# Performance work log

Hardware: AMD Instinct MI355X
Metric: run time of the kernel (lower is better)

Reference implementation:

```python
import jax, jax.numpy as jnp
import numpy as np

B = 8192          # batch of scenes
H = 20            # human_num
O = 10            # other_robot_num
IN = 13           # input_dim
SELF = 6          # self_state_dim
AG = IN - SELF    # agent_state_dim = 7
E1, E2 = 256, 128 # wr_dims / wh_dims
HID = 32          # hardcoded hidden_channels in Graphgnn
FIN = 128         # final_state_dim
P1, P2, P3 = 256, 128, 1  # planning_dims
NE = 8            # number of hetero edge types
# edge-type index convention:
# 0 robot->human, 1 human->robot, 2 other->robot, 3 robot->other,
# 4 other->human, 5 human->other, 6 human->human, 7 other->other


def setup_inputs() -> dict:
    key = jax.random.key(0)
    ks = iter(jax.random.split(key, 40))
    def nrm(shape, scale=0.05):
        return jax.random.normal(next(ks), shape, jnp.float32) * scale
    inp = {}
    inp["state"] = jax.random.normal(next(ks), (B, H + O, IN), jnp.float32)
    inp["dropout"] = 0  # unused by forward (kept for signature fidelity)
    # w_r: SELF -> E1 -> E2 (last_relu=True)
    inp["wr_W0"] = nrm((SELF, E1)); inp["wr_b0"] = nrm((E1,))
    inp["wr_W1"] = nrm((E1, E2));   inp["wr_b1"] = nrm((E2,))
    # w_h: AG -> E1 -> E2
    inp["wh_W0"] = nrm((AG, E1));   inp["wh_b0"] = nrm((E1,))
    inp["wh_W1"] = nrm((E1, E2));   inp["wh_b1"] = nrm((E2,))
    # w_o: AG -> E1 -> E2
    inp["wo_W0"] = nrm((AG, E1));   inp["wo_b0"] = nrm((E1,))
    inp["wo_W1"] = nrm((E1, E2));   inp["wo_b1"] = nrm((E2,))
    # per-edge-type GraphConv params (PyG GraphConv: lin_rel has bias, lin_root has none)
    inp["c1_relW"]  = nrm((NE, E2, HID)); inp["c1_relb"]  = nrm((NE, HID))
    inp["c1_rootW"] = nrm((NE, E2, HID))
    inp["c2_relW"]  = nrm((NE, HID, FIN)); inp["c2_relb"]  = nrm((NE, FIN))
    inp["c2_rootW"] = nrm((NE, HID, FIN))
    # value_net: FIN -> P1 -> P2 -> P3 (no final relu)
    inp["v_W0"] = nrm((FIN, P1)); inp["v_b0"] = nrm((P1,))
    inp["v_W1"] = nrm((P1, P2));  inp["v_b1"] = nrm((P2,))
    inp["v_W2"] = nrm((P2, P3));  inp["v_b2"] = nrm((P3,))
    return inp


def _mlp2(x, W0, b0, W1, b1, last_relu):
    h = jax.nn.relu(x @ W0 + b0)
    h = h @ W1 + b1
    return jax.nn.relu(h) if last_relu else h


def _hetero_conv(xr, xh, xo, relW, relb, rootW):
    # xr: [B,1,D], xh: [B,H,D], xo: [B,O,D]
    # GraphConv per edge type: out_dst = lin_root(x_dst) + lin_rel(sum of src messages)
    # graph is complete bipartite (sence) / complete-minus-self (affect),
    # so aggregations are closed-form sums.
    lin  = lambda x, i: jnp.einsum('bnd,do->bno', x, relW[i]) + relb[i]
    root = lambda x, i: jnp.einsum('bnd,do->bno', x, rootW[i])
    sh = xh.sum(axis=1, keepdims=True)  # [B,1,D] sum over humans
    so = xo.sum(axis=1, keepdims=True)  # [B,1,D] sum over other robots
    # robot receives: human->robot (1), other->robot (2)
    out_r = lin(sh, 1) + root(xr, 1) + lin(so, 2) + root(xr, 2)
    # human receives: robot->human (0), other->human (4), human->human (6)
    out_h = (lin(xr, 0) + root(xh, 0)
             + lin(so, 4) + root(xh, 4)
             + lin(sh - xh, 6) + root(xh, 6))
    # other receives: robot->other (3), human->other (5), other->other (7)
    out_o = (lin(xr, 3) + root(xo, 3)
             + lin(sh, 5) + root(xo, 5)
             + lin(so - xo, 7) + root(xo, 7))
    return out_r, out_h, out_o


def reference(state, dropout,
              wr_W0, wr_b0, wr_W1, wr_b1,
              wh_W0, wh_b0, wh_W1, wh_b1,
              wo_W0, wo_b0, wo_W1, wo_b1,
              c1_relW, c1_relb, c1_rootW,
              c2_relW, c2_relb, c2_rootW,
              v_W0, v_b0, v_W1, v_b1, v_W2, v_b2):
    self_state = state[:, 0, :SELF]          # [B, SELF]
    human_states = state[:, :H, SELF:]       # [B, H, AG]
    other_states = state[:, H:, SELF:]       # [B, O, AG]
    er = _mlp2(self_state, wr_W0, wr_b0, wr_W1, wr_b1, True)[:, None, :]  # [B,1,E2]
    eh = _mlp2(human_states, wh_W0, wh_b0, wh_W1, wh_b1, True)            # [B,H,E2]
    eo = _mlp2(other_states, wo_W0, wo_b0, wo_W1, wo_b1, True)            # [B,O,E2]
    r, h, o = _hetero_conv(er, eh, eo, c1_relW, c1_relb, c1_rootW)
    r, h, o = jax.nn.relu(r), jax.nn.relu(h), jax.nn.relu(o)
    r, h, o = _hetero_conv(r, h, o, c2_relW, c2_relb, c2_rootW)
    r = jax.nn.relu(r)
    hr = r[:, 0, :]                           # robot node per scene, [B, FIN]
    v = jax.nn.relu(hr @ v_W0 + v_b0)
    v = jax.nn.relu(v @ v_W1 + v_b1)
    v = v @ v_W2 + v_b2                       # [B, 1]
    return v
```

## Files before the change

kernel.cpp:

```cpp
#include <hip/hip_runtime.h>
#include <hip/hip_bf16.h>
#include <stdint.h>

#define BATCH 8192
#define NSTATE 30
#define DIN 13
#define E1 256
#define E2 128

typedef short bf16x8 __attribute__((ext_vector_type(8)));
typedef float f32x4 __attribute__((ext_vector_type(4)));
typedef __bf16 bf16x2_t __attribute__((ext_vector_type(2)));

__device__ __forceinline__ unsigned short f2b(float f) {
    return __builtin_bit_cast(unsigned short, (__bf16)f);
}
__device__ __forceinline__ float b2f(unsigned short b) {
    return __uint_as_float((unsigned)b << 16);
}
__device__ __forceinline__ unsigned pack2(float a, float b) {
    bf16x2_t v = {(__bf16)fmaxf(a, 0.f), (__bf16)fmaxf(b, 0.f)};
    return __builtin_bit_cast(unsigned, v);
}
__device__ __forceinline__ unsigned pack2n(float a, float b) {
    bf16x2_t v = {(__bf16)a, (__bf16)b};
    return __builtin_bit_cast(unsigned, v);
}

__device__ __forceinline__ bf16x8 pin_frag(bf16x8 v) {
    uint4 u = __builtin_bit_cast(uint4, v);
    asm volatile("" : "+v"(u.x), "+v"(u.y), "+v"(u.z), "+v"(u.w));
    return __builtin_bit_cast(bf16x8, u);
}
__device__ __forceinline__ f32x4 pin_f4(f32x4 v) {
    uint4 u = __builtin_bit_cast(uint4, v);
    asm volatile("" : "+v"(u.x), "+v"(u.y), "+v"(u.z), "+v"(u.w));
    return __builtin_bit_cast(f32x4, u);
}

__device__ __forceinline__ float wcat_val(int k, int m, const float* relW, const float* rootW) {
    int part = k >> 7, c = k & 127, grp = m >> 5, mm = m & 31;
    int off = c * 32 + mm;
    if (part == 0) return (grp == 0) ? rootW[4096 + off] + rootW[8192 + off]
                        : (grp == 1) ? relW[off] : relW[3*4096 + off];
    if (part == 1) return (grp == 0) ? relW[1*4096 + off]
                        : (grp == 1) ? relW[6*4096 + off] : relW[5*4096 + off];
    return (grp == 0) ? relW[2*4096 + off]
         : (grp == 1) ? relW[4*4096 + off] : relW[7*4096 + off];
}
__device__ __forceinline__ float wc2_val(int k, int n, const float* relW, const float* rootW) {
    int grp = k >> 5, kk = k & 31;
    int off = kk * 128 + n;
    if (grp == 0) return rootW[4096 + off] + rootW[8192 + off];
    if (grp == 1) return relW[4096 + off];
    return relW[8192 + off];
}

__global__ void k_prep(const float* __restrict__ c1_relW, const float* __restrict__ c1_relb,
                       const float* __restrict__ c1_rootW,
                       const float* __restrict__ c2_relW, const float* __restrict__ c2_relb,
                       const float* __restrict__ c2_rootW,
                       const float* __restrict__ wh_W0, const float* __restrict__ wh_W1,
                       const float* __restrict__ wo_W0, const float* __restrict__ wo_W1,
                       const float* __restrict__ wr_W0, const float* __restrict__ wr_W1,
                       const float* __restrict__ v_W0, const float* __restrict__ v_W1,
                       const float* __restrict__ b0h, const float* __restrict__ b0o,
                       const float* __restrict__ b0r,
                       float* __restrict__ bcat, float* __restrict__ bc2,
                       unsigned short* __restrict__ W0b_h, unsigned short* __restrict__ W0b_o,
                       unsigned short* __restrict__ W0b_r,
                       unsigned short* __restrict__ W1f_h, unsigned short* __restrict__ W1f_o,
                       unsigned short* __restrict__ W1f_r,
                       unsigned short* __restrict__ Mf_h, unsigned short* __restrict__ Mf_o,
                       unsigned short* __restrict__ Wcatf, unsigned short* __restrict__ Wc2f,
                       unsigned short* __restrict__ vW0f, unsigned short* __restrict__ vW1f)
{
    int gid = blockIdx.x * blockDim.x + threadIdx.x;
    int gsz = gridDim.x * blockDim.x;

    for (int i = gid; i < 96; i += gsz) {
        int grp = i >> 5, mm = i & 31;
        float v;
        if (grp == 0)      v = c1_relb[32 + mm] + c1_relb[64 + mm];
        else if (grp == 1) v = c1_relb[mm] + c1_relb[128 + mm] + c1_relb[192 + mm];
        else               v = c1_relb[96 + mm] + c1_relb[160 + mm] + c1_relb[224 + mm];
        bcat[i] = v;
    }
    for (int i = gid; i < 128; i += gsz) bc2[i] = c2_relb[128 + i] + c2_relb[256 + i];

    for (int i = gid; i < 2048; i += gsz) {
        int n = i >> 3, j = i & 7;
        W0b_h[i] = (j < 7) ? f2b(wh_W0[j * 256 + n]) : f2b(b0h[n]);
        W0b_o[i] = (j < 7) ? f2b(wo_W0[j * 256 + n]) : f2b(b0o[n]);
        W0b_r[i] = (j < 6) ? f2b(wr_W0[j * 256 + n])
                 : (j == 6) ? f2b(b0r[n]) : (unsigned short)0;
    }
    for (int i = gid; i < 32768; i += gsz) {
        int j = i & 7, l = (i >> 3) & 63, nt = (i >> 9) & 7, ks = i >> 12;
        int k = ks * 32 + (l >> 4) * 8 + j;
        int n = nt * 16 + (l & 15);
        W1f_h[i] = f2b(wh_W1[k * 128 + n]);
        W1f_o[i] = f2b(wo_W1[k * 128 + n]);
        W1f_r[i] = f2b(wr_W1[k * 128 + n]);
    }
    for (int i = gid; i < 4096; i += gsz) {
        int j = i & 7, l = (i >> 3) & 63, nt = (i >> 9) & 1, ks = i >> 10;
        int k = ks * 32 + (l >> 4) * 8 + j;
        int n = nt * 16 + (l & 15);
        int i0 = k * 32 + n;
        Mf_h[i] = f2b(c1_rootW[i0] + c1_rootW[4*4096 + i0] + c1_rootW[6*4096 + i0] - c1_relW[6*4096 + i0]);
        Mf_o[i] = f2b(c1_rootW[3*4096 + i0] + c1_rootW[5*4096 + i0] + c1_rootW[7*4096 + i0] - c1_relW[7*4096 + i0]);
    }
    for (int i = gid; i < 36864; i += gsz) {
        int j = i & 7, l = (i >> 3) & 63, rem = i >> 9;
        int nt = rem % 6, ks = rem / 6;
        int k = ks * 32 + (l >> 4) * 8 + j;
        int n = nt * 16 + (l & 15);
        Wcatf[i] = f2b(wcat_val(k, n, c1_relW, c1_rootW));
    }
    for (int i = gid; i < 12288; i += gsz) {
        int j = i & 7, l = (i >> 3) & 63, rem = i >> 9;
        int nt = rem & 7, ks = rem >> 3;
        int k = ks * 32 + (l >> 4) * 8 + j;
        int n = nt * 16 + (l & 15);
        Wc2f[i] = f2b(wc2_val(k, n, c2_relW, c2_rootW));
    }
    for (int i = gid; i < 32768; i += gsz) {
        int j = i & 7, l = (i >> 3) & 63, rem = i >> 9;
        int nt = rem & 15, ks = rem >> 4;
        int k = ks * 32 + (l >> 4) * 8 + j;
        int n = nt * 16 + (l & 15);
        vW0f[i] = f2b(v_W0[k * 256 + n]);
    }
    for (int i = gid; i < 32768; i += gsz) {
        int j = i & 7, l = (i >> 3) & 63, rem = i >> 9;
        int nt = rem & 7, ks = rem >> 3;
        int k = ks * 32 + (l >> 4) * 8 + j;
        int n = nt * 16 + (l & 15);
        vW1f[i] = f2b(v_W1[k * 128 + n]);
    }
}

#define SM_W0   0
#define SM_MF   4096
#define SM_W1   12288
#define SM_B1   78848
#define SM_HS   79360
#define SM_SZ   (79360 + 8 * 16 * 264 * 2)

template<int NPB, int NODE0, int INOFF, int INDIM, bool TAIL>
__device__ __forceinline__ void mlp_blockE(
    int blkrow0, const float* __restrict__ state,
    const unsigned short* __restrict__ W0b_g,
    const unsigned short* __restrict__ W1f_g, const float* __restrict__ b1,
    const unsigned short* __restrict__ Mf_g,
    unsigned short* __restrict__ tR, float* __restrict__ sumB,
    unsigned short* __restrict__ eR, char* smem)
{
    unsigned short* W0s = (unsigned short*)(smem + SM_W0);
    unsigned short* Mfs = (unsigned short*)(smem + SM_MF);
    unsigned short* W1s = (unsigned short*)(smem + SM_W1);
    float* b1s          = (float*)(smem + SM_B1);

    const int t = threadIdx.x;
    const int lane = t & 63;
    const int w = t >> 6;
    const int l15 = lane & 15;
    const int quad = lane >> 4;
    const int R0 = blkrow0 + w * 128;
    unsigned short* hw = (unsigned short*)(smem + SM_HS) + w * (16 * 264);
    unsigned short* ew = hw;

    if (t < 256) ((uint4*)W0s)[t] = ((const uint4*)W0b_g)[t];
    if (t >= 256 && t < 384) b1s[t - 256] = b1[t - 256];
    #pragma unroll
    for (int i = 0; i < 8; ++i)
        ((uint4*)W1s)[t + 512 * i] = ((const uint4*)W1f_g)[t + 512 * i];
    if constexpr (TAIL)
        ((uint4*)Mfs)[t] = ((const uint4*)Mf_g)[t];
    __syncthreads();

    bf16x8 wreg[32];
    #pragma unroll
    for (int ks = 0; ks < 8; ++ks)
        #pragma unroll
        for (int nt = 0; nt < 4; ++nt)
            wreg[ks * 4 + nt] =
                pin_frag(*(const bf16x8*)(W1s + ((ks * 8 + nt) * 64 + lane) * 8));

    f32x4 bias1[8];
    #pragma unroll
    for (int nt = 0; nt < 8; ++nt) {
        float4 bb = *(const float4*)(b1s + nt * 16 + quad * 4);
        bias1[nt] = pin_f4((f32x4){bb.x, bb.y, bb.z, bb.w});
    }

    float s0 = 0.f, s1 = 0.f;
    int bcur = R0 / NPB;

    float xf[INDIM];
    #pragma unroll 1
    for (int dummy = 0; dummy < 1; ++dummy) {
        if (quad == 0) {
            int grow = R0 + l15;
            int b = grow / NPB;
            int n = grow - b * NPB + NODE0;
            const float* xp = state + ((size_t)b * NSTATE + n) * DIN + INOFF;
            #pragma unroll
            for (int j = 0; j < INDIM; ++j) xf[j] = xp[j];
        }
    }

    for (int sub = 0; sub < 8; ++sub) {
        const int wrow0 = R0 + sub * 16;

        bf16x8 bx = {};
        if (quad == 0) {
            #pragma unroll
            for (int j = 0; j < INDIM; ++j)
                bx[j] = (short)f2b(xf[j]);
            bx[INDIM] = (short)0x3F80;
        }
        if (sub < 7 && quad == 0) {
            int grow = wrow0 + 16 + l15;
            int b = grow / NPB;
            int n = grow - b * NPB + NODE0;
            const float* xp = state + ((size_t)b * NSTATE + n) * DIN + INOFF;
            #pragma unroll
            for (int j = 0; j < INDIM; ++j) xf[j] = xp[j];
        }

        #pragma unroll
        for (int nt = 0; nt < 16; ++nt) {
            bf16x8 aw = {};
            if (quad == 0)
                aw = *(const bf16x8*)(W0s + (nt * 16 + l15) * 8);
            f32x4 c = {0.f, 0.f, 0.f, 0.f};
            c = __builtin_amdgcn_mfma_f32_16x16x32_bf16(aw, bx, c, 0, 0, 0);
            uint2 pv = {pack2(c[0], c[1]), pack2(c[2], c[3])};
            *(uint2*)(hw + l15 * 264 + nt * 16 + quad * 4) = pv;
        }

        f32x4 acc[8];
        #pragma unroll
        for (int nt = 0; nt < 8; ++nt) acc[nt] = bias1[nt];
        #pragma unroll
        for (int ks = 0; ks < 8; ++ks) {
            bf16x8 bh = *(const bf16x8*)(hw + l15 * 264 + ks * 32 + quad * 8);
            #pragma unroll
            for (int nt = 0; nt < 8; ++nt) {
                bf16x8 aw = (nt < 4)
                    ? wreg[ks * 4 + nt]
                    : *(const bf16x8*)(W1s + ((ks * 8 + nt) * 64 + lane) * 8);
                acc[nt] = __builtin_amdgcn_mfma_f32_16x16x32_bf16(aw, bh, acc[nt], 0, 0, 0);
            }
        }

        if constexpr (TAIL) {
            __asm__ __volatile__("s_waitcnt lgkmcnt(0)" ::: "memory");
            #pragma unroll
            for (int nt = 0; nt < 8; ++nt) {
                uint2 pv = {pack2(acc[nt][0], acc[nt][1]), pack2(acc[nt][2], acc[nt][3])};
                *(uint2*)(ew + l15 * 136 + nt * 16 + quad * 4) = pv;
            }

            f32x4 tacc[2] = {{0.f,0.f,0.f,0.f},{0.f,0.f,0.f,0.f}};
            #pragma unroll
            for (int ks = 0; ks < 4; ++ks) {
                bf16x8 ae = *(const bf16x8*)(ew + l15 * 136 + ks * 32 + quad * 8);
                #pragma unroll
                for (int nt = 0; nt < 2; ++nt) {
                    bf16x8 bm = *(const bf16x8*)(Mfs + ((ks * 2 + nt) * 64 + lane) * 8);
                    tacc[nt] = __builtin_amdgcn_mfma_f32_16x16x32_bf16(bm, ae, tacc[nt], 0, 0, 0);
                }
            }
            #pragma unroll
            for (int nt = 0; nt < 2; ++nt) {
                uint2 pv = {pack2n(tacc[nt][0], tacc[nt][1]), pack2n(tacc[nt][2], tacc[nt][3])};
                *(uint2*)(tR + (size_t)(wrow0 + l15) * 32 + nt * 16 + quad * 4) = pv;
            }

            #pragma unroll
            for (int r = 0; r < 16; ++r) {
                int b = (wrow0 + r) / NPB;
                if (b != bcur) {
                    bool interior = (bcur * NPB >= R0) && ((bcur + 1) * NPB <= R0 + 128);
                    float* dst = sumB + (size_t)bcur * 128 + 2 * lane;
                    if (interior) { dst[0] = s0; dst[1] = s1; }
                    else { atomicAdd(dst, s0); atomicAdd(dst + 1, s1); }
                    s0 = 0.f; s1 = 0.f; bcur = b;
                }
                unsigned v = *(const unsigned*)(ew + r * 136 + lane * 2);
                s0 += b2f((unsigned short)v);
                s1 += b2f((unsigned short)(v >> 16));
            }
            if (sub == 7) {
                bool interior = (bcur * NPB >= R0) && ((bcur + 1) * NPB <= R0 + 128);
                float* dst = sumB + (size_t)bcur * 128 + 2 * lane;
                if (interior) { dst[0] = s0; dst[1] = s1; }
                else { atomicAdd(dst, s0); atomicAdd(dst + 1, s1); }
            }
        } else {
            #pragma unroll
            for (int nt = 0; nt < 8; ++nt) {
                uint2 pv = {pack2(acc[nt][0], acc[nt][1]), pack2(acc[nt][2], acc[nt][3])};
                *(uint2*)(eR + (size_t)(wrow0 + l15) * 128 + nt * 16 + quad * 4) = pv;
            }
        }
        __asm__ __volatile__("" ::: "memory");
    }
}

__global__ __launch_bounds__(512, 2) void k_mlpE(
    const float* __restrict__ state,
    const unsigned short* __restrict__ W0b_h,
    const unsigned short* __restrict__ W1f_h, const float* __restrict__ b1_h,
    const unsigned short* __restrict__ Mf_h, unsigned short* __restrict__ tR_h,
    float* __restrict__ shB,
    const unsigned short* __restrict__ W0b_o,
    const unsigned short* __restrict__ W1f_o, const float* __restrict__ b1_o,
    const unsigned short* __restrict__ Mf_o, unsigned short* __restrict__ tR_o,
    float* __restrict__ soB,
    const unsigned short* __restrict__ W0b_r,
    const unsigned short* __restrict__ W1f_r, const float* __restrict__ b1_r,
    unsigned short* __restrict__ eR)
{
    __shared__ __align__(16) char smem[SM_SZ];
    int bid = blockIdx.x;
    if (bid < 160)
        mlp_blockE<20, 0, 6, 7, true>(bid * 1024, state, W0b_h, W1f_h, b1_h,
                                      Mf_h, tR_h, shB, nullptr, smem);
    else if (bid < 240)
        mlp_blockE<10, 20, 6, 7, true>((bid - 160) * 1024, state, W0b_o, W1f_o, b1_o,
                                       Mf_o, tR_o, soB, nullptr, smem);
    else
        mlp_blockE<1, 0, 0, 6, false>((bid - 240) * 1024, state, W0b_r, W1f_r, b1_r,
                                      nullptr, nullptr, nullptr, eR, smem);
}

__global__ __launch_bounds__(256, 2) void k_tail(
    const unsigned short* __restrict__ eR,
    const float* __restrict__ shB, const float* __restrict__ soB,
    const unsigned short* __restrict__ tR_h, const unsigned short* __restrict__ tR_o,
    const unsigned short* __restrict__ Wcatf, const float* __restrict__ bcat,
    const unsigned short* __restrict__ Wc2f, const float* __restrict__ bc2,
    const unsigned short* __restrict__ vW0f, const float* __restrict__ vb0,
    const unsigned short* __restrict__ vW1f, const float* __restrict__ vb1,
    const float* __restrict__ vW2, const float* __restrict__ vb2,
    float* __restrict__ out)
{
    __shared__ __align__(16) char sm[33024];
    unsigned short* Ub  = (unsigned short*)(sm);
    unsigned short* V1b = (unsigned short*)(sm);
    unsigned short* Vb  = (unsigned short*)(sm + 12800);
    float* chL          = (float*)(sm + 16128);
    float* coL          = (float*)(sm + 18176);
    unsigned short* Hb  = (unsigned short*)(sm + 20224);
    float* V2b          = (float*)(sm + 24576);

    const int t = threadIdx.x, lane = t & 63, w = t >> 6;
    const int l15 = lane & 15, quad = lane >> 4;
    const int b0 = blockIdx.x * 16;
    const int rowb = quad * 4;

    {
        int b = t >> 4, q = t & 15;
        ((uint4*)(Ub + b * 400))[q] = ((const uint4*)(eR + (size_t)(b0 + b) * 128))[q];
    }
    for (int idx = t; idx < 4096; idx += 256) {
        int b = idx >> 8, kk = idx & 255;
        float v = (kk < 128) ? shB[(size_t)(b0 + b) * 128 + kk]
                             : soB[(size_t)(b0 + b) * 128 + kk - 128];
        Ub[b * 400 + 128 + kk] = f2b(v);
    }
    __syncthreads();

    for (int nt = w; nt < 6; nt += 4) {
        float bias = bcat[nt * 16 + l15];
        f32x4 acc = {bias, bias, bias, bias};
        #pragma unroll
        for (int ks = 0; ks < 12; ++ks) {
            bf16x8 a = *(const bf16x8*)(Ub + l15 * 400 + ks * 32 + quad * 8);
            bf16x8 bw = *(const bf16x8*)(Wcatf + ((ks * 6 + nt) * 64 + lane) * 8);
            acc = __builtin_amdgcn_mfma_f32_16x16x32_bf16(a, bw, acc, 0, 0, 0);
        }
        int n = nt * 16 + l15;
        #pragma unroll
        for (int reg = 0; reg < 4; ++reg) {
            float v = acc[reg];
            int b = rowb + reg;
            if (n < 32)      Vb[b * 104 + n] = f2b(fmaxf(v, 0.f));
            else if (n < 64) chL[b * 32 + (n - 32)] = v;
            else             coL[b * 32 + (n - 64)] = v;
        }
    }
    __syncthreads();

    for (int idx = t; idx < 512; idx += 256) {
        int b = idx >> 5, m = idx & 31;
        float ch = chL[b * 32 + m];
        const unsigned short* p = tR_h + (size_t)(b0 + b) * 20 * 32 + m;
        float s = 0.f;
        #pragma unroll
        for (int n = 0; n < 20; ++n) s += fmaxf(ch + b2f(p[n * 32]), 0.f);
        Vb[b * 104 + 32 + m] = f2b(s);
        float co = coL[b * 32 + m];
        const unsigned short* p2 = tR_o + (size_t)(b0 + b) * 10 * 32 + m;
        float s2 = 0.f;
        #pragma unroll
        for (int n = 0; n < 10; ++n) s2 += fmaxf(co + b2f(p2[n * 32]), 0.f);
        Vb[b * 104 + 64 + m] = f2b(s2);
    }
    __syncthreads();

    {
        f32x4 acc[2];
        #pragma unroll
        for (int q = 0; q < 2; ++q) {
            int nt = w + q * 4;
            float bias = bc2[nt * 16 + l15];
            acc[q] = (f32x4){bias, bias, bias, bias};
        }
        #pragma unroll
        for (int ks = 0; ks < 3; ++ks) {
            bf16x8 a = *(const bf16x8*)(Vb + l15 * 104 + ks * 32 + quad * 8);
            #pragma unroll
            for (int q = 0; q < 2; ++q) {
                int nt = w + q * 4;
                bf16x8 bw = *(const bf16x8*)(Wc2f + ((ks * 8 + nt) * 64 + lane) * 8);
                acc[q] = __builtin_amdgcn_mfma_f32_16x16x32_bf16(a, bw, acc[q], 0, 0, 0);
            }
        }
        #pragma unroll
        for (int q = 0; q < 2; ++q) {
            int nt = w + q * 4;
            #pragma unroll
            for (int reg = 0; reg < 4; ++reg)
                Hb[(rowb + reg) * 136 + nt * 16 + l15] = f2b(fmaxf(acc[q][reg], 0.f));
        }
    }
    __syncthreads();

    {
        f32x4 acc[4];
        #pragma unroll
        for (int q = 0; q < 4; ++q) {
            int nt = w + q * 4;
            float bias = vb0[nt * 16 + l15];
            acc[q] = (f32x4){bias, bias, bias, bias};
        }
        #pragma unroll
        for (int ks = 0; ks < 4; ++ks) {
            bf16x8 a = *(const bf16x8*)(Hb + l15 * 136 + ks * 32 + quad * 8);
            #pragma unroll
            for (int q = 0; q < 4; ++q) {
                int nt = w + q * 4;
                bf16x8 bw = *(const bf16x8*)(vW0f + ((ks * 16 + nt) * 64 + lane) * 8);
                acc[q] = __builtin_amdgcn_mfma_f32_16x16x32_bf16(a, bw, acc[q], 0, 0, 0);
            }
        }
        __syncthreads();
        #pragma unroll
        for (int q = 0; q < 4; ++q) {
            int nt = w + q * 4;
            #pragma unroll
            for (int reg = 0; reg < 4; ++reg)
                V1b[(rowb + reg) * 264 + nt * 16 + l15] = f2b(fmaxf(acc[q][reg], 0.f));
        }
    }
    __syncthreads();

    {
        f32x4 acc[2];
        #pragma unroll
        for (int q = 0; q < 2; ++q) {
            int nt = w + q * 4;
            float bias = vb1[nt * 16 + l15];
            acc[q] = (f32x4){bias, bias, bias, bias};
        }
        #pragma unroll
        for (int ks = 0; ks < 8; ++ks) {
            bf16x8 a = *(const bf16x8*)(V1b + l15 * 264 + ks * 32 + quad * 8);
            #pragma unroll
            for (int q = 0; q < 2; ++q) {
                int nt = w + q * 4;
                bf16x8 bw = *(const bf16x8*)(vW1f + ((ks * 8 + nt) * 64 + lane) * 8);
                acc[q] = __builtin_amdgcn_mfma_f32_16x16x32_bf16(a, bw, acc[q], 0, 0, 0);
            }
        }
        #pragma unroll
        for (int q = 0; q < 2; ++q) {
            int nt = w + q * 4;
            #pragma unroll
            for (int reg = 0; reg < 4; ++reg)
                V2b[(rowb + reg) * 132 + nt * 16 + l15] = fmaxf(acc[q][reg], 0.f);
        }
    }
    __syncthreads();

    if (t < 128) {
        int b = t >> 3, j = t & 7;
        float v = 0.f;
        #pragma unroll
        for (int k = 0; k < 16; ++k)
            v = fmaf(V2b[b * 132 + j * 16 + k], vW2[j * 16 + k], v);
        v += __shfl_down(v, 4, 8);
        v += __shfl_down(v, 2, 8);
        v += __shfl_down(v, 1, 8);
        if (j == 0) out[b0 + b] = v + vb2[0];
    }
}

extern "C" void kernel_launch(void* const* d_in, const int* in_sizes, int n_in,
                              void* d_out, int out_size, void* d_ws, size_t ws_size,
                              hipStream_t stream)
{
    const float* state   = (const float*)d_in[0];
    const float* wr_W0   = (const float*)d_in[2];
    const float* wr_b0   = (const float*)d_in[3];
    const float* wr_W1   = (const float*)d_in[4];
    const float* wr_b1   = (const float*)d_in[5];
    const float* wh_W0   = (const float*)d_in[6];
    const float* wh_b0   = (const float*)d_in[7];
    const float* wh_W1   = (const float*)d_in[8];
    const float* wh_b1   = (const float*)d_in[9];
    const float* wo_W0   = (const float*)d_in[10];
    const float* wo_b0   = (const float*)d_in[11];
    const float* wo_W1   = (const float*)d_in[12];
    const float* wo_b1   = (const float*)d_in[13];
    const float* c1_relW = (const float*)d_in[14];
    const float* c1_relb = (const float*)d_in[15];
    const float* c1_rootW= (const float*)d_in[16];
    const float* c2_relW = (const float*)d_in[17];
    const float* c2_relb = (const float*)d_in[18];
    const float* c2_rootW= (const float*)d_in[19];
    const float* v_W0    = (const float*)d_in[20];
    const float* v_b0    = (const float*)d_in[21];
    const float* v_W1    = (const float*)d_in[22];
    const float* v_b1    = (const float*)d_in[23];
    const float* v_W2    = (const float*)d_in[24];
    const float* v_b2    = (const float*)d_in[25];

    char* ws = (char*)d_ws;
    size_t off = 0;
    auto alloc = [&](size_t bytes) -> char* {
        char* p = ws + off;
        off = (off + bytes + 255) & ~(size_t)255;
        return p;
    };
    float* shB  = (float*)alloc((size_t)BATCH * 128 * 4);
    float* soB  = (float*)alloc((size_t)BATCH * 128 * 4);
    unsigned short* tR_h = (unsigned short*)alloc((size_t)163840 * 32 * 2);
    unsigned short* tR_o = (unsigned short*)alloc((size_t)81920 * 32 * 2);
    unsigned short* eR   = (unsigned short*)alloc((size_t)BATCH * 128 * 2);
    float* bcat = (float*)alloc(96 * 4);
    float* bc2  = (float*)alloc(128 * 4);
    unsigned short* W0b_h = (unsigned short*)alloc(2048 * 2);
    unsigned short* W0b_o = (unsigned short*)alloc(2048 * 2);
    unsigned short* W0b_r = (unsigned short*)alloc(2048 * 2);
    unsigned short* W1f_h = (unsigned short*)alloc(32768 * 2);
    unsigned short* W1f_o = (unsigned short*)alloc(32768 * 2);
    unsigned short* W1f_r = (unsigned short*)alloc(32768 * 2);
    unsigned short* Mf_h  = (unsigned short*)alloc(4096 * 2);
    unsigned short* Mf_o  = (unsigned short*)alloc(4096 * 2);
    unsigned short* Wcatf = (unsigned short*)alloc(36864 * 2);
    unsigned short* Wc2f  = (unsigned short*)alloc(12288 * 2);
    unsigned short* vW0f  = (unsigned short*)alloc(32768 * 2);
    unsigned short* vW1f  = (unsigned short*)alloc(32768 * 2);
    (void)ws_size; (void)in_sizes; (void)n_in; (void)out_size;

    hipMemsetAsync(shB, 0, (size_t)2 * BATCH * 128 * 4, stream);

    k_prep<<<256, 256, 0, stream>>>(c1_relW, c1_relb, c1_rootW, c2_relW, c2_relb, c2_rootW,
                                    wh_W0, wh_W1, wo_W0, wo_W1, wr_W0, wr_W1, v_W0, v_W1,
                                    wh_b0, wo_b0, wr_b0,
                                    bcat, bc2, W0b_h, W0b_o, W0b_r, W1f_h, W1f_o, W1f_r,
                                    Mf_h, Mf_o, Wcatf, Wc2f, vW0f, vW1f);

    k_mlpE<<<248, 512, 0, stream>>>(state,
                                    W0b_h, W1f_h, wh_b1, Mf_h, tR_h, shB,
                                    W0b_o, W1f_o, wo_b1, Mf_o, tR_o, soB,
                                    W0b_r, W1f_r, wr_b1, eR);

    k_tail<<<512, 256, 0, stream>>>(eR, shB, soB, tR_h, tR_o,
                                    Wcatf, bcat, Wc2f, bc2, vW0f, v_b0, vW1f, v_b1,
                                    v_W2, v_b2, (float*)d_out);
}
```

Baseline: 169.7 us.

## Chain MFMA outputs through registers by permuting weight K-ordering

```diff
diff --git a/kernel.cpp b/kernel.cpp
--- a/kernel.cpp
+++ b/kernel.cpp
@@ -27,11 +27,6 @@
     return __builtin_bit_cast(unsigned, v);
 }
 
-__device__ __forceinline__ bf16x8 pin_frag(bf16x8 v) {
-    uint4 u = __builtin_bit_cast(uint4, v);
-    asm volatile("" : "+v"(u.x), "+v"(u.y), "+v"(u.z), "+v"(u.w));
-    return __builtin_bit_cast(bf16x8, u);
-}
 __device__ __forceinline__ f32x4 pin_f4(f32x4 v) {
     uint4 u = __builtin_bit_cast(uint4, v);
     asm volatile("" : "+v"(u.x), "+v"(u.y), "+v"(u.z), "+v"(u.w));
@@ -97,17 +92,17 @@
     }
     for (int i = gid; i < 32768; i += gsz) {
         int j = i & 7, l = (i >> 3) & 63, nt = (i >> 9) & 7, ks = i >> 12;
-        int k = ks * 32 + (l >> 4) * 8 + j;
+        int kk = ((j >> 2) * 8 + ks) * 16 + (l >> 4) * 4 + (j & 3);
         int n = nt * 16 + (l & 15);
-        W1f_h[i] = f2b(wh_W1[k * 128 + n]);
-        W1f_o[i] = f2b(wo_W1[k * 128 + n]);
-        W1f_r[i] = f2b(wr_W1[k * 128 + n]);
+        W1f_h[i] = f2b(wh_W1[kk * 128 + n]);
+        W1f_o[i] = f2b(wo_W1[kk * 128 + n]);
+        W1f_r[i] = f2b(wr_W1[kk * 128 + n]);
     }
     for (int i = gid; i < 4096; i += gsz) {
         int j = i & 7, l = (i >> 3) & 63, nt = (i >> 9) & 1, ks = i >> 10;
-        int k = ks * 32 + (l >> 4) * 8 + j;
+        int kk = ((j >> 2) * 4 + ks) * 16 + (l >> 4) * 4 + (j & 3);
         int n = nt * 16 + (l & 15);
-        int i0 = k * 32 + n;
+        int i0 = kk * 32 + n;
         Mf_h[i] = f2b(c1_rootW[i0] + c1_rootW[4*4096 + i0] + c1_rootW[6*4096 + i0] - c1_relW[6*4096 + i0]);
         Mf_o[i] = f2b(c1_rootW[3*4096 + i0] + c1_rootW[5*4096 + i0] + c1_rootW[7*4096 + i0] - c1_relW[7*4096 + i0]);
     }
@@ -144,9 +139,9 @@
 #define SM_W0   0
 #define SM_MF   4096
 #define SM_W1   12288
-#define SM_B1   78848
-#define SM_HS   79360
-#define SM_SZ   (79360 + 8 * 16 * 264 * 2)
+#define SM_B1   77824
+#define SM_HS   78336
+#define SM_SZ   (78336 + 8 * 16 * 136 * 2)
 
 template<int NPB, int NODE0, int INOFF, int INDIM, bool TAIL>
 __device__ __forceinline__ void mlp_blockE(
@@ -168,8 +163,7 @@
     const int l15 = lane & 15;
     const int quad = lane >> 4;
     const int R0 = blkrow0 + w * 128;
-    unsigned short* hw = (unsigned short*)(smem + SM_HS) + w * (16 * 264);
-    unsigned short* ew = hw;
+    unsigned short* ew = (unsigned short*)(smem + SM_HS) + w * (16 * 136);
 
     if (t < 256) ((uint4*)W0s)[t] = ((const uint4*)W0b_g)[t];
     if (t >= 256 && t < 384) b1s[t - 256] = b1[t - 256];
@@ -179,14 +173,6 @@
     if constexpr (TAIL)
         ((uint4*)Mfs)[t] = ((const uint4*)Mf_g)[t];
     __syncthreads();
-
-    bf16x8 wreg[32];
-    #pragma unroll
-    for (int ks = 0; ks < 8; ++ks)
-        #pragma unroll
-        for (int nt = 0; nt < 4; ++nt)
-            wreg[ks * 4 + nt] =
-                pin_frag(*(const bf16x8*)(W1s + ((ks * 8 + nt) * 64 + lane) * 8));
 
     f32x4 bias1[8];
     #pragma unroll
@@ -230,15 +216,25 @@
             for (int j = 0; j < INDIM; ++j) xf[j] = xp[j];
         }
 
+        f32x4 a1[16];
         #pragma unroll
         for (int nt = 0; nt < 16; ++nt) {
             bf16x8 aw = {};
             if (quad == 0)
                 aw = *(const bf16x8*)(W0s + (nt * 16 + l15) * 8);
             f32x4 c = {0.f, 0.f, 0.f, 0.f};
-            c = __builtin_amdgcn_mfma_f32_16x16x32_bf16(aw, bx, c, 0, 0, 0);
-            uint2 pv = {pack2(c[0], c[1]), pack2(c[2], c[3])};
-            *(uint2*)(hw + l15 * 264 + nt * 16 + quad * 4) = pv;
+            a1[nt] = __builtin_amdgcn_mfma_f32_16x16x32_bf16(aw, bx, c, 0, 0, 0);
+        }
+
+        bf16x8 bh[8];
+        #pragma unroll
+        for (int ks = 0; ks < 8; ++ks) {
+            uint4 u;
+            u.x = pack2(a1[ks][0], a1[ks][1]);
+            u.y = pack2(a1[ks][2], a1[ks][3]);
+            u.z = pack2(a1[ks + 8][0], a1[ks + 8][1]);
+            u.w = pack2(a1[ks + 8][2], a1[ks + 8][3]);
+            bh[ks] = __builtin_bit_cast(bf16x8, u);
         }
 
         f32x4 acc[8];
@@ -246,28 +242,31 @@
         for (int nt = 0; nt < 8; ++nt) acc[nt] = bias1[nt];
         #pragma unroll
         for (int ks = 0; ks < 8; ++ks) {
-            bf16x8 bh = *(const bf16x8*)(hw + l15 * 264 + ks * 32 + quad * 8);
             #pragma unroll
             for (int nt = 0; nt < 8; ++nt) {
-                bf16x8 aw = (nt < 4)
-                    ? wreg[ks * 4 + nt]
-                    : *(const bf16x8*)(W1s + ((ks * 8 + nt) * 64 + lane) * 8);
-                acc[nt] = __builtin_amdgcn_mfma_f32_16x16x32_bf16(aw, bh, acc[nt], 0, 0, 0);
-            }
-        }
+                bf16x8 aw = *(const bf16x8*)(W1s + ((ks * 8 + nt) * 64 + lane) * 8);
+                acc[nt] = __builtin_amdgcn_mfma_f32_16x16x32_bf16(aw, bh[ks], acc[nt], 0, 0, 0);
+            }
+        }
+
+        uint2 pv[8];
+        #pragma unroll
+        for (int nt = 0; nt < 8; ++nt)
+            pv[nt] = (uint2){pack2(acc[nt][0], acc[nt][1]), pack2(acc[nt][2], acc[nt][3])};
 
         if constexpr (TAIL) {
             __asm__ __volatile__("s_waitcnt lgkmcnt(0)" ::: "memory");
             #pragma unroll
-            for (int nt = 0; nt < 8; ++nt) {
-                uint2 pv = {pack2(acc[nt][0], acc[nt][1]), pack2(acc[nt][2], acc[nt][3])};
-                *(uint2*)(ew + l15 * 136 + nt * 16 + quad * 4) = pv;
-            }
+            for (int nt = 0; nt < 8; ++nt)
+                *(uint2*)(ew + l15 * 136 + nt * 16 + quad * 4) = pv[nt];
 
             f32x4 tacc[2] = {{0.f,0.f,0.f,0.f},{0.f,0.f,0.f,0.f}};
             #pragma unroll
             for (int ks = 0; ks < 4; ++ks) {
-                bf16x8 ae = *(const bf16x8*)(ew + l15 * 136 + ks * 32 + quad * 8);
+                uint4 ua;
+                ua.x = pv[ks].x; ua.y = pv[ks].y;
+                ua.z = pv[ks + 4].x; ua.w = pv[ks + 4].y;
+                bf16x8 ae = __builtin_bit_cast(bf16x8, ua);
                 #pragma unroll
                 for (int nt = 0; nt < 2; ++nt) {
                     bf16x8 bm = *(const bf16x8*)(Mfs + ((ks * 2 + nt) * 64 + lane) * 8);
@@ -276,8 +275,8 @@
             }
             #pragma unroll
             for (int nt = 0; nt < 2; ++nt) {
-                uint2 pv = {pack2n(tacc[nt][0], tacc[nt][1]), pack2n(tacc[nt][2], tacc[nt][3])};
-                *(uint2*)(tR + (size_t)(wrow0 + l15) * 32 + nt * 16 + quad * 4) = pv;
+                uint2 tv = {pack2n(tacc[nt][0], tacc[nt][1]), pack2n(tacc[nt][2], tacc[nt][3])};
+                *(uint2*)(tR + (size_t)(wrow0 + l15) * 32 + nt * 16 + quad * 4) = tv;
             }
 
             #pragma unroll
@@ -302,10 +301,8 @@
             }
         } else {
             #pragma unroll
-            for (int nt = 0; nt < 8; ++nt) {
-                uint2 pv = {pack2(acc[nt][0], acc[nt][1]), pack2(acc[nt][2], acc[nt][3])};
-                *(uint2*)(eR + (size_t)(wrow0 + l15) * 128 + nt * 16 + quad * 4) = pv;
-            }
+            for (int nt = 0; nt < 8; ++nt)
+                *(uint2*)(eR + (size_t)(wrow0 + l15) * 128 + nt * 16 + quad * 4) = pv[nt];
         }
         __asm__ __volatile__("" ::: "memory");
     }
```

Result: faster. 164.6 us (-3.0%).
